# Kernel optimization log

Hardware: AMD Instinct MI355X
Metric: run time of the kernel (lower is better)

## Reference

```python
import jax, jax.numpy as jnp
import numpy as np

E, C, CAP = 16, 256, 4  # experts, channels per expert, capacity expansion

def setup_inputs() -> dict:
    key = jax.random.key(0)
    k1, k2, k3, k4, k5 = jax.random.split(key, 5)
    B, L = 8, 1024
    x = jax.random.normal(k1, (B, E * C, L), dtype=jnp.float32)
    # Conv1d weights (kernel_size=1 squeezed): [out_ch, in_ch_per_group]
    W1 = jax.random.normal(k2, (E * C * CAP, C), dtype=jnp.float32) * (1.0 / np.sqrt(C))
    b1 = jax.random.normal(k3, (E * C * CAP,), dtype=jnp.float32) * 0.01
    W2 = jax.random.normal(k4, (E * C, C * CAP), dtype=jnp.float32) * (1.0 / np.sqrt(C * CAP))
    b2 = jax.random.normal(k5, (E * C,), dtype=jnp.float32) * 0.01
    return {"x": x, "W1": W1, "b1": b1, "W2": W2, "b2": b2}

def reference(x, W1, b1, W2, b2):
    # Grouped 1x1 Conv1d == block-diagonal per-expert matmul over length axis.
    B, CE, L = x.shape
    xr = x.reshape(B, E, C, L)                       # [B,E,C,L]
    W1r = W1.reshape(E, C * CAP, C)                  # [E,F,C], F = C*CAP
    W2r = W2.reshape(E, C, C * CAP)                  # [E,C,F]
    h = jnp.einsum('becl,efc->befl', xr, W1r) + b1.reshape(1, E, C * CAP, 1)
    h = jax.nn.silu(h)                               # [B,E,F,L]
    y = jnp.einsum('befl,ecf->becl', h, W2r) + b2.reshape(1, E, C, 1)
    return y.reshape(B, E * C, L)
```

## Files before the change

kernel.cpp:

```cpp
#include <hip/hip_runtime.h>
#include <hip/hip_bf16.h>
#include <stdint.h>

#define EE 16
#define CC 256
#define FF 1024
#define LL 1024
#define BB 8
#define TL 128
#define FC 32
#define NCH 32
#define HSTR 56

typedef __bf16 bf16x8 __attribute__((ext_vector_type(8)));
typedef __bf16 bf16x4 __attribute__((ext_vector_type(4)));
typedef float  f32x4  __attribute__((ext_vector_type(4)));

__device__ __forceinline__ f32x4 mfma16(bf16x8 a, bf16x8 b, f32x4 c) {
    return __builtin_amdgcn_mfma_f32_16x16x32_bf16(a, b, c, 0, 0, 0);
}

__device__ __forceinline__ void gld_lds16(const __bf16* g, __bf16* l) {
    __builtin_amdgcn_global_load_lds(
        (const __attribute__((address_space(1))) void*)g,
        (__attribute__((address_space(3))) void*)l, 16, 0, 0);
}

__global__ void cvt_w1(const float* __restrict__ W1, __bf16* __restrict__ ws) {
    int g = blockIdx.x * blockDim.x + threadIdx.x;
    int f  = g & 31;
    int cg = (g >> 5) & 31;
    int ec = g >> 10;
    int ch = ec & 31, e = ec >> 5;
    const float* s = W1 + ((size_t)(e * 1024 + ch * 32 + f)) * 256 + cg * 8;
    float4 v0 = *(const float4*)s;
    float4 v1 = *(const float4*)(s + 4);
    bf16x8 o;
    o[0]=(__bf16)v0.x; o[1]=(__bf16)v0.y; o[2]=(__bf16)v0.z; o[3]=(__bf16)v0.w;
    o[4]=(__bf16)v1.x; o[5]=(__bf16)v1.y; o[6]=(__bf16)v1.z; o[7]=(__bf16)v1.w;
    *(bf16x8*)(ws + (size_t)g * 8) = o;
}
__global__ void cvt_w2(const float* __restrict__ W2, __bf16* __restrict__ ws) {
    int g = blockIdx.x * blockDim.x + threadIdx.x;
    int c  = g & 255;
    int fg = (g >> 8) & 3;
    int ec = g >> 10;
    int ch = ec & 31, e = ec >> 5;
    const float* s = W2 + ((size_t)(e * 256 + c)) * 1024 + ch * 32 + fg * 8;
    float4 v0 = *(const float4*)s;
    float4 v1 = *(const float4*)(s + 4);
    bf16x8 o;
    o[0]=(__bf16)v0.x; o[1]=(__bf16)v0.y; o[2]=(__bf16)v0.z; o[3]=(__bf16)v0.w;
    o[4]=(__bf16)v1.x; o[5]=(__bf16)v1.y; o[6]=(__bf16)v1.z; o[7]=(__bf16)v1.w;
    *(bf16x8*)(ws + (size_t)g * 8) = o;
}

__global__ __launch_bounds__(1024, 4)
void experts_kernel(const float* __restrict__ x,
                    const __bf16* __restrict__ w1ws,
                    const float* __restrict__ b1,
                    const __bf16* __restrict__ w2ws,
                    const float* __restrict__ b2,
                    float* __restrict__ out)
{
    __shared__ __align__(16) __bf16 sW1[3][FC * CC];
    __shared__ __align__(16) __bf16 sW2[3][CC * FC];
    __shared__ __align__(16) __bf16 sH[2][8][16 * HSTR];

    const int tid  = threadIdx.x;
    const int lane = tid & 63;
    const int w    = tid >> 6;
    const int l15  = lane & 15, q4 = lane >> 4;
    const int lt   = w >> 1;
    const int fh   = w & 1;

    const int bid  = blockIdx.x;
    const int e    = ((bid & 7) << 1) | ((bid >> 3) & 1);
    const int rest = bid >> 4;
    const int bb   = rest & 7;
    const int l0   = (rest >> 3) * TL;
    const int lb   = l0 + 16 * lt;

    const __bf16* w1c = w1ws + (size_t)e * NCH * (FC * CC);
    const __bf16* w2c = w2ws + (size_t)e * NCH * (CC * FC);
    const int slice = w * 512;

    gld_lds16(w1c + 0 * 8192 + slice + lane * 8, &sW1[0][slice]);
    gld_lds16(w2c + 0 * 8192 + slice + lane * 8, &sW2[0][slice]);
    gld_lds16(w1c + 1 * 8192 + slice + lane * 8, &sW1[1][slice]);
    gld_lds16(w2c + 1 * 8192 + slice + lane * 8, &sW2[1][slice]);

    bf16x8 xf[8];
    {
        const float* xp = x + ((size_t)(bb * EE + e) * CC) * LL + lb + l15;
        #pragma unroll
        for (int ks = 0; ks < 8; ++ks) {
            bf16x8 f;
            #pragma unroll
            for (int t = 0; t < 8; ++t)
                f[t] = (__bf16)xp[(size_t)(32 * ks + 8 * q4 + t) * LL];
            xf[ks] = f;
        }
    }

    f32x4 accY[8];
    #pragma unroll
    for (int t = 0; t < 8; ++t) accY[t] = f32x4{0.f, 0.f, 0.f, 0.f};

    __syncthreads();

    int cur = 0;
    #pragma unroll 1
    for (int ch = 0; ch < NCH; ++ch) {
        const int p = ch & 1;

        const float4 bv = *(const float4*)(b1 + e * FF + ch * FC + 16 * fh + 4 * q4);
        f32x4 acc1 = f32x4{0.f, 0.f, 0.f, 0.f};
        const __bf16* a1base = &sW1[cur][(16 * fh + l15) * 8];
        #pragma unroll
        for (int ks = 0; ks < 8; ++ks) {
            bf16x8 a = *(const bf16x8*)(a1base + (4 * ks + q4) * 256);
            acc1 = mfma16(a, xf[ks], acc1);
        }
        {
            bf16x4 hv;
            #pragma unroll
            for (int r = 0; r < 4; ++r) {
                float v = acc1[r] + ((const float*)&bv)[r];
                hv[r] = (__bf16)(v / (1.0f + __expf(-v)));
            }
            *(bf16x4*)(&sH[p][lt][l15 * HSTR + 16 * fh + 4 * q4]) = hv;
        }

        __syncthreads();

        if (ch + 2 < NCH) {
            int nxt = cur + 2; if (nxt >= 3) nxt -= 3;
            gld_lds16(w1c + (size_t)(ch + 2) * 8192 + slice + lane * 8, &sW1[nxt][slice]);
            gld_lds16(w2c + (size_t)(ch + 2) * 8192 + slice + lane * 8, &sW2[nxt][slice]);
        }

        {
            bf16x8 hf = *(const bf16x8*)(&sH[p][lt][l15 * HSTR + 8 * q4]);
            const __bf16* a2base = &sW2[cur][(128 * fh + l15) * 8];
            #pragma unroll
            for (int t = 0; t < 8; ++t) {
                bf16x8 a = *(const bf16x8*)(a2base + (q4 * 256 + 16 * t) * 8);
                accY[t] = mfma16(a, hf, accY[t]);
            }
        }
        ++cur; if (cur == 3) cur = 0;
    }

    float* outp = out + ((size_t)(bb * EE + e) * CC) * LL + lb + l15;
    #pragma unroll
    for (int t = 0; t < 8; ++t) {
        const int c0 = 128 * fh + 16 * t + 4 * q4;
        const float4 b2v = *(const float4*)(b2 + e * CC + c0);
        #pragma unroll
        for (int r = 0; r < 4; ++r) {
            __builtin_nontemporal_store(accY[t][r] + ((const float*)&b2v)[r],
                                        outp + (size_t)(c0 + r) * LL);
        }
    }
}

extern "C" void kernel_launch(void* const* d_in, const int* in_sizes, int n_in,
                              void* d_out, int out_size, void* d_ws, size_t ws_size,
                              hipStream_t stream)
{
    const float* x  = (const float*)d_in[0];
    const float* W1 = (const float*)d_in[1];
    const float* b1 = (const float*)d_in[2];
    const float* W2 = (const float*)d_in[3];
    const float* b2 = (const float*)d_in[4];
    float* out = (float*)d_out;

    const size_t nW1 = (size_t)EE * FF * CC;
    const size_t nW2 = (size_t)EE * CC * FF;
    __bf16* w1bf = (__bf16*)d_ws;
    __bf16* w2bf = w1bf + nW1;

    const int ng = (int)(nW1 / 8);
    cvt_w1<<<dim3(ng / 256), dim3(256), 0, stream>>>(W1, w1bf);
    cvt_w2<<<dim3(ng / 256), dim3(256), 0, stream>>>(W2, w2bf);

    experts_kernel<<<dim3(BB * EE * (LL / TL)), dim3(1024), 0, stream>>>(
        x, w1bf, b1, w2bf, b2, out);
}
```

Before: 467.4 us.

## Warp-specialize expert MLP into producer/consumer waves and fuse weight conversion

Splits the 16 waves into 8 producer waves that compute the first GEMM plus SiLU into shared memory and 8 consumer waves that run the second GEMM one chunk behind. The stages are software-pipelined across the chunk loop, and each wave now covers 32 columns instead of 16. The two weight-conversion kernels are merged into one launch that transposes through LDS, so global reads and writes are coalesced. This trades stage parallelism for an extra loop iteration and uneven register and MFMA load between wave roles, and uses s_setprio hints.

```diff
diff --git a/kernel.cpp b/kernel.cpp
--- a/kernel.cpp
+++ b/kernel.cpp
@@ -10,7 +10,7 @@
 #define TL 128
 #define FC 32
 #define NCH 32
-#define HSTR 56
+#define HSTR 40
 
 typedef __bf16 bf16x8 __attribute__((ext_vector_type(8)));
 typedef __bf16 bf16x4 __attribute__((ext_vector_type(4)));
@@ -26,33 +26,55 @@
         (__attribute__((address_space(3))) void*)l, 16, 0, 0);
 }
 
-__global__ void cvt_w1(const float* __restrict__ W1, __bf16* __restrict__ ws) {
-    int g = blockIdx.x * blockDim.x + threadIdx.x;
-    int f  = g & 31;
-    int cg = (g >> 5) & 31;
-    int ec = g >> 10;
-    int ch = ec & 31, e = ec >> 5;
-    const float* s = W1 + ((size_t)(e * 1024 + ch * 32 + f)) * 256 + cg * 8;
-    float4 v0 = *(const float4*)s;
-    float4 v1 = *(const float4*)(s + 4);
-    bf16x8 o;
-    o[0]=(__bf16)v0.x; o[1]=(__bf16)v0.y; o[2]=(__bf16)v0.z; o[3]=(__bf16)v0.w;
-    o[4]=(__bf16)v1.x; o[5]=(__bf16)v1.y; o[6]=(__bf16)v1.z; o[7]=(__bf16)v1.w;
-    *(bf16x8*)(ws + (size_t)g * 8) = o;
-}
-__global__ void cvt_w2(const float* __restrict__ W2, __bf16* __restrict__ ws) {
-    int g = blockIdx.x * blockDim.x + threadIdx.x;
-    int c  = g & 255;
-    int fg = (g >> 8) & 3;
-    int ec = g >> 10;
-    int ch = ec & 31, e = ec >> 5;
-    const float* s = W2 + ((size_t)(e * 256 + c)) * 1024 + ch * 32 + fg * 8;
-    float4 v0 = *(const float4*)s;
-    float4 v1 = *(const float4*)(s + 4);
-    bf16x8 o;
-    o[0]=(__bf16)v0.x; o[1]=(__bf16)v0.y; o[2]=(__bf16)v0.z; o[3]=(__bf16)v0.w;
-    o[4]=(__bf16)v1.x; o[5]=(__bf16)v1.y; o[6]=(__bf16)v1.z; o[7]=(__bf16)v1.w;
-    *(bf16x8*)(ws + (size_t)g * 8) = o;
+__global__ __launch_bounds__(256)
+void cvt_both(const float* __restrict__ W1, const float* __restrict__ W2,
+              __bf16* __restrict__ ws1, __bf16* __restrict__ ws2)
+{
+    __shared__ __align__(16) __bf16 ls[8448];
+    const int t = threadIdx.x;
+    const int bid = blockIdx.x;
+    if (bid < 512) {
+        const float* src = W1 + (size_t)bid * 8192;
+        #pragma unroll
+        for (int i = 0; i < 8; ++i) {
+            const int p = t + 256 * i;
+            const float4 v = *(const float4*)(src + 4 * p);
+            const int f = p >> 6, c4 = p & 63;
+            const int cg = c4 >> 1, j0 = (c4 & 1) * 4;
+            bf16x4 o;
+            o[0] = (__bf16)v.x; o[1] = (__bf16)v.y; o[2] = (__bf16)v.z; o[3] = (__bf16)v.w;
+            *(bf16x4*)(ls + cg * 264 + f * 8 + j0) = o;
+        }
+        __syncthreads();
+        __bf16* dst = ws1 + (size_t)bid * 8192;
+        #pragma unroll
+        for (int i = 0; i < 4; ++i) {
+            const int G = t + 256 * i;
+            const int cg = G >> 5, f = G & 31;
+            *(bf16x8*)(dst + (size_t)G * 8) = *(const bf16x8*)(ls + cg * 264 + f * 8);
+        }
+    } else {
+        const int tile = bid - 512;
+        const float* src = W2 + (size_t)(tile >> 5) * 262144 + (tile & 31) * 32;
+        #pragma unroll
+        for (int i = 0; i < 8; ++i) {
+            const int u = t + 256 * i;
+            const int c = u >> 3, col4 = u & 7;
+            const float4 v = *(const float4*)(src + (size_t)c * 1024 + col4 * 4);
+            const int fg = col4 >> 1, j0 = (col4 & 1) * 4;
+            bf16x4 o;
+            o[0] = (__bf16)v.x; o[1] = (__bf16)v.y; o[2] = (__bf16)v.z; o[3] = (__bf16)v.w;
+            *(bf16x4*)(ls + fg * 2056 + c * 8 + j0) = o;
+        }
+        __syncthreads();
+        __bf16* dst = ws2 + (size_t)tile * 8192;
+        #pragma unroll
+        for (int i = 0; i < 4; ++i) {
+            const int G = t + 256 * i;
+            const int fg = G >> 8, c = G & 255;
+            *(bf16x8*)(dst + (size_t)G * 8) = *(const bf16x8*)(ls + fg * 2056 + c * 8);
+        }
+    }
 }
 
 __global__ __launch_bounds__(1024, 4)
@@ -65,24 +87,25 @@
 {
     __shared__ __align__(16) __bf16 sW1[3][FC * CC];
     __shared__ __align__(16) __bf16 sW2[3][CC * FC];
-    __shared__ __align__(16) __bf16 sH[2][8][16 * HSTR];
+    __shared__ __align__(16) __bf16 sH[2][4][32 * HSTR];
 
     const int tid  = threadIdx.x;
     const int lane = tid & 63;
     const int w    = tid >> 6;
     const int l15  = lane & 15, q4 = lane >> 4;
-    const int lt   = w >> 1;
+    const bool prod = (w < 8);
     const int fh   = w & 1;
+    const int lw   = (w & 7) >> 1;
 
     const int bid  = blockIdx.x;
     const int e    = ((bid & 7) << 1) | ((bid >> 3) & 1);
     const int rest = bid >> 4;
     const int bb   = rest & 7;
     const int l0   = (rest >> 3) * TL;
-    const int lb   = l0 + 16 * lt;
-
-    const __bf16* w1c = w1ws + (size_t)e * NCH * (FC * CC);
-    const __bf16* w2c = w2ws + (size_t)e * NCH * (CC * FC);
+    const int lb   = l0 + 32 * lw;
+
+    const __bf16* w1c = w1ws + (size_t)e * (NCH * FC * CC);
+    const __bf16* w2c = w2ws + (size_t)e * (NCH * CC * FC);
     const int slice = w * 512;
 
     gld_lds16(w1c + 0 * 8192 + slice + lane * 8, &sW1[0][slice]);
@@ -90,77 +113,102 @@
     gld_lds16(w1c + 1 * 8192 + slice + lane * 8, &sW1[1][slice]);
     gld_lds16(w2c + 1 * 8192 + slice + lane * 8, &sW2[1][slice]);
 
-    bf16x8 xf[8];
-    {
+    f32x4 st[2][8];
+    if (prod) {
         const float* xp = x + ((size_t)(bb * EE + e) * CC) * LL + lb + l15;
         #pragma unroll
-        for (int ks = 0; ks < 8; ++ks) {
-            bf16x8 f;
-            #pragma unroll
-            for (int t = 0; t < 8; ++t)
-                f[t] = (__bf16)xp[(size_t)(32 * ks + 8 * q4 + t) * LL];
-            xf[ks] = f;
-        }
-    }
-
-    f32x4 accY[8];
-    #pragma unroll
-    for (int t = 0; t < 8; ++t) accY[t] = f32x4{0.f, 0.f, 0.f, 0.f};
+        for (int lt = 0; lt < 2; ++lt) {
+            #pragma unroll
+            for (int ks = 0; ks < 8; ++ks) {
+                bf16x8 f;
+                #pragma unroll
+                for (int u = 0; u < 8; ++u)
+                    f[u] = (__bf16)xp[(size_t)(32 * ks + 8 * q4 + u) * LL + 16 * lt];
+                st[lt][ks] = __builtin_bit_cast(f32x4, f);
+            }
+        }
+    } else {
+        #pragma unroll
+        for (int lt = 0; lt < 2; ++lt)
+            #pragma unroll
+            for (int u = 0; u < 8; ++u) st[lt][u] = f32x4{0.f, 0.f, 0.f, 0.f};
+    }
 
     __syncthreads();
 
-    int cur = 0;
+    int rp = 0;
     #pragma unroll 1
-    for (int ch = 0; ch < NCH; ++ch) {
-        const int p = ch & 1;
-
-        const float4 bv = *(const float4*)(b1 + e * FF + ch * FC + 16 * fh + 4 * q4);
-        f32x4 acc1 = f32x4{0.f, 0.f, 0.f, 0.f};
-        const __bf16* a1base = &sW1[cur][(16 * fh + l15) * 8];
-        #pragma unroll
-        for (int ks = 0; ks < 8; ++ks) {
-            bf16x8 a = *(const bf16x8*)(a1base + (4 * ks + q4) * 256);
-            acc1 = mfma16(a, xf[ks], acc1);
-        }
-        {
-            bf16x4 hv;
-            #pragma unroll
-            for (int r = 0; r < 4; ++r) {
-                float v = acc1[r] + ((const float*)&bv)[r];
-                hv[r] = (__bf16)(v / (1.0f + __expf(-v)));
-            }
-            *(bf16x4*)(&sH[p][lt][l15 * HSTR + 16 * fh + 4 * q4]) = hv;
-        }
-
-        __syncthreads();
-
-        if (ch + 2 < NCH) {
-            int nxt = cur + 2; if (nxt >= 3) nxt -= 3;
-            gld_lds16(w1c + (size_t)(ch + 2) * 8192 + slice + lane * 8, &sW1[nxt][slice]);
-            gld_lds16(w2c + (size_t)(ch + 2) * 8192 + slice + lane * 8, &sW2[nxt][slice]);
-        }
-
-        {
-            bf16x8 hf = *(const bf16x8*)(&sH[p][lt][l15 * HSTR + 8 * q4]);
-            const __bf16* a2base = &sW2[cur][(128 * fh + l15) * 8];
-            #pragma unroll
-            for (int t = 0; t < 8; ++t) {
-                bf16x8 a = *(const bf16x8*)(a2base + (q4 * 256 + 16 * t) * 8);
-                accY[t] = mfma16(a, hf, accY[t]);
-            }
-        }
-        ++cur; if (cur == 3) cur = 0;
-    }
-
-    float* outp = out + ((size_t)(bb * EE + e) * CC) * LL + lb + l15;
-    #pragma unroll
-    for (int t = 0; t < 8; ++t) {
-        const int c0 = 128 * fh + 16 * t + 4 * q4;
-        const float4 b2v = *(const float4*)(b2 + e * CC + c0);
-        #pragma unroll
-        for (int r = 0; r < 4; ++r) {
-            __builtin_nontemporal_store(accY[t][r] + ((const float*)&b2v)[r],
-                                        outp + (size_t)(c0 + r) * LL);
+    for (int ch = 0; ch <= NCH; ++ch) {
+        const int rq = (rp >= 1) ? rp - 1 : 2;
+
+        if (prod) {
+            if (ch < NCH) {
+                const float4 bv = *(const float4*)(b1 + e * FF + ch * FC + 16 * fh + 4 * q4);
+                f32x4 a0 = f32x4{0.f, 0.f, 0.f, 0.f};
+                f32x4 a1 = f32x4{0.f, 0.f, 0.f, 0.f};
+                const __bf16* a1base = &sW1[rp][(16 * fh + l15) * 8];
+                __builtin_amdgcn_s_setprio(1);
+                #pragma unroll
+                for (int ks = 0; ks < 8; ++ks) {
+                    bf16x8 a = *(const bf16x8*)(a1base + (4 * ks + q4) * 256);
+                    a0 = mfma16(a, __builtin_bit_cast(bf16x8, st[0][ks]), a0);
+                    a1 = mfma16(a, __builtin_bit_cast(bf16x8, st[1][ks]), a1);
+                }
+                __builtin_amdgcn_s_setprio(0);
+                __bf16* hrow = &sH[ch & 1][lw][l15 * HSTR + 16 * fh + 4 * q4];
+                bf16x4 hv;
+                #pragma unroll
+                for (int r = 0; r < 4; ++r) {
+                    float v = a0[r] + ((const float*)&bv)[r];
+                    hv[r] = (__bf16)(v / (1.0f + __expf(-v)));
+                }
+                *(bf16x4*)hrow = hv;
+                #pragma unroll
+                for (int r = 0; r < 4; ++r) {
+                    float v = a1[r] + ((const float*)&bv)[r];
+                    hv[r] = (__bf16)(v / (1.0f + __expf(-v)));
+                }
+                *(bf16x4*)(hrow + 16 * HSTR) = hv;
+            }
+        } else if (ch >= 1) {
+            const __bf16* hbase = &sH[(ch & 1) ^ 1][lw][l15 * HSTR + 8 * q4];
+            bf16x8 h0 = *(const bf16x8*)(hbase);
+            bf16x8 h1 = *(const bf16x8*)(hbase + 16 * HSTR);
+            const __bf16* a2base = &sW2[rq][(128 * fh + l15) * 8];
+            __builtin_amdgcn_s_setprio(1);
+            #pragma unroll
+            for (int u = 0; u < 8; ++u) {
+                bf16x8 a = *(const bf16x8*)(a2base + (q4 * 256 + 16 * u) * 8);
+                st[0][u] = mfma16(a, h0, st[0][u]);
+                st[1][u] = mfma16(a, h1, st[1][u]);
+            }
+            __builtin_amdgcn_s_setprio(0);
+        }
+
+        if (ch < NCH) {
+            __syncthreads();
+            if (ch + 2 < NCH) {
+                gld_lds16(w1c + (size_t)(ch + 2) * 8192 + slice + lane * 8, &sW1[rq][slice]);
+                gld_lds16(w2c + (size_t)(ch + 2) * 8192 + slice + lane * 8, &sW2[rq][slice]);
+            }
+        }
+        rp = (rp >= 2) ? 0 : rp + 1;
+    }
+
+    if (!prod) {
+        float* outp = out + ((size_t)(bb * EE + e) * CC) * LL + lb + l15;
+        #pragma unroll
+        for (int u = 0; u < 8; ++u) {
+            const int c0 = 128 * fh + 16 * u + 4 * q4;
+            const float4 b2v = *(const float4*)(b2 + e * CC + c0);
+            #pragma unroll
+            for (int lt = 0; lt < 2; ++lt) {
+                #pragma unroll
+                for (int r = 0; r < 4; ++r)
+                    __builtin_nontemporal_store(
+                        st[lt][u][r] + ((const float*)&b2v)[r],
+                        outp + (size_t)(c0 + r) * LL + 16 * lt);
+            }
         }
     }
 }
@@ -177,13 +225,10 @@
     float* out = (float*)d_out;
 
     const size_t nW1 = (size_t)EE * FF * CC;
-    const size_t nW2 = (size_t)EE * CC * FF;
     __bf16* w1bf = (__bf16*)d_ws;
     __bf16* w2bf = w1bf + nW1;
 
-    const int ng = (int)(nW1 / 8);
-    cvt_w1<<<dim3(ng / 256), dim3(256), 0, stream>>>(W1, w1bf);
-    cvt_w2<<<dim3(ng / 256), dim3(256), 0, stream>>>(W2, w2bf);
+    cvt_both<<<dim3(1024), dim3(256), 0, stream>>>(W1, W2, w1bf, w2bf);
 
     experts_kernel<<<dim3(BB * EE * (LL / TL)), dim3(1024), 0, stream>>>(
         x, w1bf, b1, w2bf, b2, out);
```

Measured after the change: 455.4 us. 2.6% less time.
